# Optimization experiments

Measured on AMD Instinct MI355X. Metric: run time of the kernel, lower is better.

## Reference

```python
import jax, jax.numpy as jnp
import numpy as np

B, N, D_ATOM, HID, L = 32, 64, 5, 256, 9
E = N * N
F_E = 2 * HID + 2  # [h_i, h_j, d^2, edge_attr]


def _gather(x, idx):
    # x: (B, N, D), idx: (B, E) -> (B, E, D)
    return jax.vmap(lambda a, i: a[i])(x, idx)


def _segsum(data, idx, n):
    # per-batch unsorted segment sum over destination node idx
    return jax.vmap(lambda d, i: jax.ops.segment_sum(d, i, num_segments=n))(data, idx)


def _safe_dist(diff):
    # sqrt of squared norm, safe at 0 (masked self-edges) for grads
    return jnp.sqrt(jnp.maximum(jnp.sum(diff ** 2, axis=-1, keepdims=True), 1e-12))


def _remove_mean(x, mask):
    n = jnp.sum(mask, axis=1, keepdims=True)
    return (x - jnp.sum(x, axis=1, keepdims=True) / n) * mask


def setup_inputs() -> dict:
    key = jax.random.key(0)
    ks = iter(jax.random.split(key, 32))

    def W(shape):
        return jax.random.normal(next(ks), shape, jnp.float32) * 0.02

    x_in = jax.random.normal(next(ks), (B, N, 3), jnp.float32)
    h_in = jax.random.uniform(next(ks), (B, N, D_ATOM), dtype=jnp.float32)
    t = jax.random.uniform(next(ks), (B, N, 1), dtype=jnp.float32)
    ii, jj = jnp.meshgrid(jnp.arange(N), jnp.arange(N), indexing='ij')
    edges = jnp.stack([ii.reshape(-1), jj.reshape(-1)], axis=-1).astype(jnp.int32)  # (E,2) all pairs
    edge_indices = jnp.broadcast_to(edges[None], (B, E, 2))
    node_mask = jnp.ones((B, N, 1), jnp.float32)
    em = (edges[:, 0] != edges[:, 1]).astype(jnp.float32)[:, None]  # mask self-edges
    edge_mask = jnp.broadcast_to(em[None], (B, E, 1))
    params = dict(
        win_w=W((D_ATOM + 1, HID)), win_b=jnp.zeros((HID,), jnp.float32),
        wout_w=W((HID, D_ATOM + 1)), wout_b=jnp.zeros((D_ATOM + 1,), jnp.float32),
        we_w1=W((L, F_E, HID)), we_b1=jnp.zeros((L, HID), jnp.float32),
        we_w2=W((L, HID, HID)), we_b2=jnp.zeros((L, HID), jnp.float32),
        attn_w=W((L, HID, 1)), attn_b=jnp.zeros((L, 1), jnp.float32),
        wh_w1=W((L, 2 * HID, HID)), wh_b1=jnp.zeros((L, HID), jnp.float32),
        wh_w2=W((L, HID, HID)), wh_b2=jnp.zeros((L, HID), jnp.float32),
        wx_w1=W((L, F_E, HID)), wx_b1=jnp.zeros((L, HID), jnp.float32),
        wx_w2=W((L, HID, HID)), wx_b2=jnp.zeros((L, HID), jnp.float32),
        wx_w3=W((L, HID, 1)),
    )
    return dict(x_in=x_in, h_in=h_in, t=t, node_mask=node_mask, edge_mask=edge_mask,
                edge_indices=edge_indices, **params)


def reference(x_in, h_in, t, node_mask, edge_mask, edge_indices,
              win_w, win_b, wout_w, wout_b,
              we_w1, we_b1, we_w2, we_b2, attn_w, attn_b,
              wh_w1, wh_b1, wh_w2, wh_b2,
              wx_w1, wx_b1, wx_w2, wx_b2, wx_w3):
    idx_i = edge_indices[..., 0]
    idx_j = edge_indices[..., 1]
    # fixed edge attribute: initial pairwise distance
    d_in = _safe_dist(_gather(x_in, idx_i) - _gather(x_in, idx_j)) * edge_mask
    h0 = jnp.concatenate([h_in, t], axis=-1) @ win_w + win_b

    def block(carry, p):
        x, h = carry
        ew1, eb1, ew2, eb2, aw, ab, hw1, hb1, hw2, hb2, xw1, xb1, xw2, xb2, xw3 = p
        diff = (_gather(x, idx_i) - _gather(x, idx_j)) * edge_mask  # (B,E,3)
        d = _safe_dist(diff)  # (B,E,1)
        feat = jnp.concatenate([_gather(h, idx_i), _gather(h, idx_j), d ** 2, d_in], axis=-1) * edge_mask
        # edge MLP + attention gate, aggregated to node i
        m = jax.nn.silu(jax.nn.silu(feat @ ew1 + eb1) @ ew2 + eb2)
        em_agg = _segsum(jax.nn.sigmoid(m @ aw + ab) * m, idx_i, N)
        h_new = (h + (jax.nn.silu(jnp.concatenate([h, em_agg], axis=-1) @ hw1 + hb1) @ hw2 + hb2)) * node_mask
        # coordinate update (no bias on last layer)
        s = jax.nn.silu(jax.nn.silu(feat @ xw1 + xb1) @ xw2 + xb2) @ xw3  # (B,E,1)
        x_new = (x + _segsum(diff / (d + 1.0) * s, idx_i, N)) * node_mask
        return (x_new, h_new), None

    stacked = (we_w1, we_b1, we_w2, we_b2, attn_w, attn_b,
               wh_w1, wh_b1, wh_w2, wh_b2, wx_w1, wx_b1, wx_w2, wx_b2, wx_w3)
    (x, h), _ = jax.lax.scan(block, (x_in, h0), stacked)
    x_out = _remove_mean((x - x_in) * node_mask, node_mask)
    h_out = ((h @ wout_w + wout_b) * node_mask)[..., :-1]
    return jnp.concatenate([x_out, h_out], axis=-1)
```

## Files before the change

kernel.cpp:

```cpp
#include <hip/hip_runtime.h>
#include <hip/hip_bf16.h>
#include <math.h>


#define NB   32
#define NN   64
#define EPB  4096
#define HID  256
#define NL   9

typedef __attribute__((ext_vector_type(8))) short bfrag;
typedef __attribute__((ext_vector_type(4))) float f32x4;
typedef __attribute__((ext_vector_type(2))) float f32x2;

__device__ __forceinline__ float fast_rcp(float x) { return __builtin_amdgcn_rcpf(x); }
__device__ __forceinline__ float silu_f(float x) { return x * fast_rcp(1.f + __expf(-x)); }
__device__ __forceinline__ float sigm_f(float x) { return fast_rcp(1.f + __expf(-x)); }
__device__ __forceinline__ ushort bf16rne(float x) {
    unsigned u = __builtin_bit_cast(unsigned, x);
    u = (u + 0x7fffu + ((u >> 16) & 1u)) >> 16;
    return (ushort)u;
}
__device__ __forceinline__ float bf16tof(ushort h) {
    unsigned u = ((unsigned)h) << 16;
    return __builtin_bit_cast(float, u);
}
__device__ __forceinline__ unsigned pk2(f32x2 v) {
    float2 f; f.x = v.x; f.y = v.y;
    __hip_bfloat162 t = __float22bfloat162_rn(f);
    unsigned u;
    __builtin_memcpy(&u, &t, 4);
    return u;
}
__device__ __forceinline__ f32x2 fma2(f32x2 a, f32x2 b, f32x2 c) {
    return __builtin_elementwise_fma(a, b, c);
}
__device__ __forceinline__ f32x4 fma4(f32x4 a, f32x4 b, f32x4 c) {
    return __builtin_elementwise_fma(a, b, c);
}
__device__ __forceinline__ f32x2 silu2(f32x2 v) {
    f32x2 e = { __expf(-v.x), __expf(-v.y) };
    f32x2 d = e + (f32x2){1.f, 1.f};
    f32x2 r = { fast_rcp(d.x), fast_rcp(d.y) };
    return v * r;
}
__device__ __forceinline__ f32x4 silu4(f32x4 v) {
    f32x4 e = { __expf(-v.x), __expf(-v.y), __expf(-v.z), __expf(-v.w) };
    f32x4 d = e + (f32x4){1.f, 1.f, 1.f, 1.f};
    f32x4 r = { fast_rcp(d.x), fast_rcp(d.y), fast_rcp(d.z), fast_rcp(d.w) };
    return v * r;
}

__global__ void edm_k0_pre(const float* __restrict__ x_in, const float* __restrict__ h_in,
                           const float* __restrict__ t_in,
                           const float* __restrict__ win_w, const float* __restrict__ win_b,
                           float* __restrict__ h0, float* __restrict__ din_ws,
                           float* __restrict__ x0)
{
    int blk = blockIdx.x, tid = threadIdx.x;
    if (blk < NB * NN) {
        int node = blk;
        float acc = win_b[tid];
        #pragma unroll
        for (int k = 0; k < 5; ++k) acc += h_in[node * 5 + k] * win_w[k * HID + tid];
        acc += t_in[node] * win_w[5 * HID + tid];
        h0[node * HID + tid] = acc;
    } else if (blk < NB * NN + 512) {
        int e = (blk - NB * NN) * 256 + tid;
        int b = e >> 12, r = e & 4095, i = r >> 6, j = r & 63;
        const float* xb = x_in + b * NN * 3;
        float d0 = xb[i*3+0] - xb[j*3+0];
        float d1 = xb[i*3+1] - xb[j*3+1];
        float d2 = xb[i*3+2] - xb[j*3+2];
        float ss = d0*d0 + d1*d1 + d2*d2;
        float d  = sqrtf(fmaxf(ss, 1e-12f));
        din_ws[e] = (i != j) ? d : 0.f;
    } else {
        int idx = (blk - (NB * NN + 512)) * 256 + tid;
        if (idx < NB * NN * 3) x0[idx] = x_in[idx];
    }
}

__global__ void edm_k5_prep(const float* __restrict__ we_w2, const float* __restrict__ wx_w2,
                            ushort* __restrict__ W2Te, ushort* __restrict__ W2Tx)
{
    __shared__ float t_s[64][65];
    int blk = blockIdx.x;
    int mat = blk / 144, rem = blk % 144, l = rem >> 4, tile = rem & 15;
    int kt = tile >> 2, nt = tile & 3;
    const float* src = (mat ? wx_w2 : we_w2) + l * HID * HID;
    ushort* dst = (mat ? W2Tx : W2Te) + l * HID * HID;
    int col = threadIdx.x & 63, rg = threadIdx.x >> 6;
    #pragma unroll
    for (int it = 0; it < 16; ++it) {
        int row = rg * 16 + it;
        t_s[row][col] = src[(kt * 64 + row) * HID + nt * 64 + col];
    }
    __syncthreads();
    #pragma unroll
    for (int it = 0; it < 16; ++it) {
        int n = rg * 16 + it;
        dst[(nt * 64 + n) * HID + kt * 64 + col] = bf16rne(t_s[col][n]);
    }
}

__global__ void edm_k5b_prep(const float* __restrict__ we_w1, const float* __restrict__ wx_w1,
                             ushort* __restrict__ W1Th, ushort* __restrict__ W1Tl)
{
    __shared__ float t_s[64][65];
    int blk = blockIdx.x;
    int tile = blk & 15, out = (blk >> 4) & 3, l = blk >> 6;
    int kt = tile >> 2, nt = tile & 3;
    const float* src = ((out >= 2) ? wx_w1 : we_w1) + l * 514 * HID + (out & 1) * 256 * HID;
    size_t doff = ((size_t)(l * 4 + out)) * HID * HID;
    ushort* dh = W1Th + doff;
    ushort* dl = W1Tl + doff;
    int col = threadIdx.x & 63, rg = threadIdx.x >> 6;
    #pragma unroll
    for (int it = 0; it < 16; ++it) {
        int row = rg * 16 + it;
        t_s[row][col] = src[(kt * 64 + row) * HID + nt * 64 + col];
    }
    __syncthreads();
    #pragma unroll
    for (int it = 0; it < 16; ++it) {
        int n = rg * 16 + it;
        float v = t_s[col][n];
        ushort h = bf16rne(v);
        float lo = v - bf16tof(h);
        dh[(nt * 64 + n) * HID + kt * 64 + col] = h;
        dl[(nt * 64 + n) * HID + kt * 64 + col] = bf16rne(lo);
    }
}

__global__ void edm_k5c_prep(const float* __restrict__ wh_w1, const float* __restrict__ wh_w2,
                             ushort* __restrict__ W3h, ushort* __restrict__ W3l,
                             ushort* __restrict__ W4h, ushort* __restrict__ W4l)
{
    __shared__ float t_s[64][65];
    int blk = blockIdx.x;
    const float* src; ushort* dh; ushort* dl; int kt, nt, Kdim;
    if (blk < 288) {
        int l = blk >> 5, tile = blk & 31;
        kt = tile >> 2; nt = tile & 3; Kdim = 512;
        src = wh_w1 + (size_t)l * 512 * HID;
        dh = W3h + (size_t)l * HID * 512;
        dl = W3l + (size_t)l * HID * 512;
    } else {
        int b2 = blk - 288;
        int l = b2 >> 4, tile = b2 & 15;
        kt = tile >> 2; nt = tile & 3; Kdim = 256;
        src = wh_w2 + (size_t)l * HID * HID;
        dh = W4h + (size_t)l * HID * HID;
        dl = W4l + (size_t)l * HID * HID;
    }
    int col = threadIdx.x & 63, rg = threadIdx.x >> 6;
    #pragma unroll
    for (int it = 0; it < 16; ++it) {
        int row = rg * 16 + it;
        t_s[row][col] = src[(size_t)(kt * 64 + row) * HID + nt * 64 + col];
    }
    __syncthreads();
    #pragma unroll
    for (int it = 0; it < 16; ++it) {
        int n = rg * 16 + it;
        float v = t_s[col][n];
        ushort h = bf16rne(v);
        float lo = v - bf16tof(h);
        dh[(size_t)(nt * 64 + n) * Kdim + kt * 64 + col] = h;
        dl[(size_t)(nt * 64 + n) * Kdim + kt * 64 + col] = bf16rne(lo);
    }
}

__global__ __launch_bounds__(256)
void edm_k1_mfma(const float* __restrict__ h,
                 const ushort* __restrict__ W1Th, const ushort* __restrict__ W1Tl,
                 const float* __restrict__ we_b1, const float* __restrict__ wx_b1,
                 const float* __restrict__ we_w2, const float* __restrict__ we_b2,
                 const float* __restrict__ attn_w, const float* __restrict__ attn_b,
                 float* __restrict__ HeA, float* __restrict__ HeB,
                 float* __restrict__ HxA, float* __restrict__ HxB,
                 float* __restrict__ self_em, int l)
{
    int tid = threadIdx.x;
    if (blockIdx.x == 512) {
        __shared__ float m1s[HID];
        __shared__ float ms[HID];
        __shared__ float wred[4];
        __shared__ float gsh;
        const float* eb1 = we_b1 + l * HID;
        m1s[tid] = silu_f(eb1[tid]);
        __syncthreads();
        const float* W2 = we_w2 + l * HID * HID;
        float acc = we_b2[l * HID + tid];
        for (int k = 0; k < HID; ++k) acc += m1s[k] * W2[k * HID + tid];
        float mv = silu_f(acc);
        ms[tid] = mv;
        float p = mv * attn_w[l * HID + tid];
        #pragma unroll
        for (int off = 32; off > 0; off >>= 1) p += __shfl_down(p, off, 64);
        if ((tid & 63) == 0) wred[tid >> 6] = p;
        __syncthreads();
        if (tid == 0) gsh = sigm_f(wred[0] + wred[1] + wred[2] + wred[3] + attn_b[l]);
        __syncthreads();
        self_em[tid] = gsh * ms[tid];
        return;
    }

    __shared__ __align__(16) ushort Ah_s[16384];
    __shared__ __align__(16) ushort Al_s[16384];

    const int cq = blockIdx.x & 3;
    const int out = (blockIdx.x >> 2) & 3;
    const int ntile = blockIdx.x >> 4;
    const int base = ntile * 64;

    {
        const int c  = tid & 31;
        const int jg = tid >> 5;
        const int k0 = c * 8;
        #pragma unroll
        for (int it = 0; it < 8; ++it) {
            int m = it * 8 + jg;
            f32x4 h0 = *(const f32x4*)&h[(base + m) * HID + k0];
            f32x4 h1 = *(const f32x4*)&h[(base + m) * HID + k0 + 4];
            uint4 phi, plo;
            {
                ushort ax = bf16rne(h0.x), ay = bf16rne(h0.y);
                phi.x = (unsigned)ax | ((unsigned)ay << 16);
                plo.x = pk2((f32x2){h0.x - bf16tof(ax), h0.y - bf16tof(ay)});
            }
            {
                ushort ax = bf16rne(h0.z), ay = bf16rne(h0.w);
                phi.y = (unsigned)ax | ((unsigned)ay << 16);
                plo.y = pk2((f32x2){h0.z - bf16tof(ax), h0.w - bf16tof(ay)});
            }
            {
                ushort ax = bf16rne(h1.x), ay = bf16rne(h1.y);
                phi.z = (unsigned)ax | ((unsigned)ay << 16);
                plo.z = pk2((f32x2){h1.x - bf16tof(ax), h1.y - bf16tof(ay)});
            }
            {
                ushort ax = bf16rne(h1.z), ay = bf16rne(h1.w);
                phi.w = (unsigned)ax | ((unsigned)ay << 16);
                plo.w = pk2((f32x2){h1.z - bf16tof(ax), h1.w - bf16tof(ay)});
            }
            unsigned off = (unsigned)(m * 256 + ((c ^ (m & 7)) * 8));
            *(uint4*)&Ah_s[off] = phi;
            *(uint4*)&Al_s[off] = plo;
        }
    }
    __syncthreads();

    const int w = tid >> 6, lane = tid & 63, quad = lane >> 4, l16 = lane & 15;
    const int col = cq * 64 + w * 16 + l16;
    const ushort* Bh = W1Th + ((size_t)(l * 4 + out)) * HID * HID + (size_t)col * HID;
    const ushort* Bl = W1Tl + ((size_t)(l * 4 + out)) * HID * HID + (size_t)col * HID;

    f32x4 acc[4];
    #pragma unroll
    for (int mt = 0; mt < 4; ++mt) acc[mt] = (f32x4){0.f, 0.f, 0.f, 0.f};

    #pragma unroll
    for (int kt = 0; kt < 8; ++kt) {
        const int kof = kt * 32 + quad * 8;
        const int ch  = (kt * 4 + quad) ^ (l16 & 7);
        bfrag bh = *(const bfrag*)&Bh[kof];
        bfrag bl = *(const bfrag*)&Bl[kof];
        bfrag ahr[4], alr[4];
        #pragma unroll
        for (int mt = 0; mt < 4; ++mt) {
            ahr[mt] = *(const bfrag*)&Ah_s[(mt * 16 + l16) * 256 + ch * 8];
            alr[mt] = *(const bfrag*)&Al_s[(mt * 16 + l16) * 256 + ch * 8];
        }
        #pragma unroll
        for (int mt = 0; mt < 4; ++mt) {
            acc[mt] = __builtin_amdgcn_mfma_f32_16x16x32_bf16(ahr[mt], bh, acc[mt], 0, 0, 0);
            acc[mt] = __builtin_amdgcn_mfma_f32_16x16x32_bf16(ahr[mt], bl, acc[mt], 0, 0, 0);
            acc[mt] = __builtin_amdgcn_mfma_f32_16x16x32_bf16(alr[mt], bh, acc[mt], 0, 0, 0);
        }
    }

    float bias = 0.f;
    if (out == 0) bias = we_b1[l * HID + col];
    else if (out == 2) bias = wx_b1[l * HID + col];
    float* dst = (out == 0) ? HeA : (out == 1) ? HeB : (out == 2) ? HxA : HxB;
    #pragma unroll
    for (int mt = 0; mt < 4; ++mt)
        #pragma unroll
        for (int r = 0; r < 4; ++r)
            dst[(base + mt * 16 + quad * 4 + r) * HID + col] = acc[mt][r] + bias;
}

__global__ __launch_bounds__(256, 4)
void edm_kb_gemm(const float* __restrict__ x_cur, float* __restrict__ x_next,
                 const float* __restrict__ HeA, const float* __restrict__ HeB,
                 const float* __restrict__ HxA, const float* __restrict__ HxB,
                 const float* __restrict__ din_ws,
                 const float* __restrict__ we_w1, const float* __restrict__ we_b1,
                 const float* __restrict__ wx_w1, const float* __restrict__ wx_b1,
                 const ushort* __restrict__ W2Te, const ushort* __restrict__ W2Tx,
                 const float* __restrict__ we_b2, const float* __restrict__ wx_b2,
                 const float* __restrict__ attn_w, const float* __restrict__ attn_b,
                 const float* __restrict__ wx_w3,
                 float* __restrict__ em_agg, int l)
{
    __shared__ __align__(16) ushort A_s[16384];
    __shared__ float red_s[256];
    __shared__ float sc_s[64];
    __shared__ float x_s[192];
    __shared__ float d2_s[64], din_s[64];

    const int tid = threadIdx.x;
    const int blk = blockIdx.x;
    const int p = blk >> 11, bi = blk & 2047, b = bi >> 6, i = bi & 63;

    if (tid < 192) x_s[tid] = x_cur[b * 192 + tid];
    __syncthreads();
    if (tid < 64) {
        int j = tid;
        float d0 = x_s[i*3+0] - x_s[j*3+0];
        float d1 = x_s[i*3+1] - x_s[j*3+1];
        float d2 = x_s[i*3+2] - x_s[j*3+2];
        float ss = d0*d0 + d1*d1 + d2*d2;
        float d  = sqrtf(fmaxf(ss, 1e-12f));
        d2_s[j]  = d * d;
        din_s[j] = din_ws[b * EPB + i * 64 + j];
    }
    __syncthreads();

    {
        const float* W1  = (p ? wx_w1 : we_w1) + l * 514 * HID;
        const float* HA  = (p ? HxA : HeA);
        const float* HB  = (p ? HxB : HeB);
        const float* b1p = (p ? wx_b1 : we_b1) + l * HID;

        const int c  = tid & 31;
        const int jg = tid >> 5;
        const int k0 = c * 8;

        f32x4 ra0 = *(const f32x4*)&HA[(b * 64 + i) * HID + k0];
        f32x4 ra1 = *(const f32x4*)&HA[(b * 64 + i) * HID + k0 + 4];
        f32x4 wa0 = *(const f32x4*)&W1[512 * HID + k0];
        f32x4 wa1 = *(const f32x4*)&W1[512 * HID + k0 + 4];
        f32x4 wb0 = *(const f32x4*)&W1[513 * HID + k0];
        f32x4 wb1 = *(const f32x4*)&W1[513 * HID + k0 + 4];
        f32x4 b10 = *(const f32x4*)&b1p[k0];
        f32x4 b11 = *(const f32x4*)&b1p[k0 + 4];
        uint4 pki;
        pki.x = pk2(silu2((f32x2){b10.x, b10.y}));
        pki.y = pk2(silu2((f32x2){b10.z, b10.w}));
        pki.z = pk2(silu2((f32x2){b11.x, b11.y}));
        pki.w = pk2(silu2((f32x2){b11.z, b11.w}));

        const float* hbp = HB + b * 64 * HID + k0;
        #pragma unroll
        for (int it = 0; it < 8; ++it) {
            int j = it * 8 + jg;
            f32x4 h0 = *(const f32x4*)&hbp[j * HID];
            f32x4 h1 = *(const f32x4*)&hbp[j * HID + 4];
            f32x2 dd = { d2_s[j], d2_s[j] };
            f32x2 dn = { din_s[j], din_s[j] };
            uint4 pkv;
            f32x2 v;
            v = fma2(dn, (f32x2){wb0.x, wb0.y},
                 fma2(dd, (f32x2){wa0.x, wa0.y},
                      (f32x2){ra0.x + h0.x, ra0.y + h0.y}));
            pkv.x = pk2(silu2(v));
            v = fma2(dn, (f32x2){wb0.z, wb0.w},
                 fma2(dd, (f32x2){wa0.z, wa0.w},
                      (f32x2){ra0.z + h0.z, ra0.w + h0.w}));
            pkv.y = pk2(silu2(v));
            v = fma2(dn, (f32x2){wb1.x, wb1.y},
                 fma2(dd, (f32x2){wa1.x, wa1.y},
                      (f32x2){ra1.x + h1.x, ra1.y + h1.y}));
            pkv.z = pk2(silu2(v));
            v = fma2(dn, (f32x2){wb1.z, wb1.w},
                 fma2(dd, (f32x2){wa1.z, wa1.w},
                      (f32x2){ra1.z + h1.z, ra1.w + h1.w}));
            pkv.w = pk2(silu2(v));
            if (j == i) pkv = pki;
            *(uint4*)&A_s[j * 256 + (unsigned)((c ^ (j & 7)) * 8)] = pkv;
        }
    }
    __syncthreads();

    const int w = tid >> 6, lane = tid & 63, quad = lane >> 4, l16 = lane & 15;
    const ushort* W2T = (p ? W2Tx : W2Te) + l * HID * HID;
    const int cb0 = w * 64 + l16;
    f32x4 acc[4][4];
    #pragma unroll
    for (int mt = 0; mt < 4; ++mt)
        #pragma unroll
        for (int nt = 0; nt < 4; ++nt) acc[mt][nt] = (f32x4){0.f, 0.f, 0.f, 0.f};

    #pragma unroll
    for (int kt = 0; kt < 8; ++kt) {
        const int kof = kt * 32 + quad * 8;
        const int ch  = (kt * 4 + quad) ^ (l16 & 7);
        bfrag bfr[4], afr[4];
        #pragma unroll
        for (int nt = 0; nt < 4; ++nt)
            bfr[nt] = *(const bfrag*)&W2T[(cb0 + nt * 16) * HID + kof];
        #pragma unroll
        for (int mt = 0; mt < 4; ++mt)
            afr[mt] = *(const bfrag*)&A_s[(mt * 16 + l16) * 256 + ch * 8];
        #pragma unroll
        for (int mt = 0; mt < 4; ++mt)
            #pragma unroll
            for (int nt = 0; nt < 4; ++nt)
                acc[mt][nt] = __builtin_amdgcn_mfma_f32_16x16x32_bf16(
                    afr[mt], bfr[nt], acc[mt][nt], 0, 0, 0);
    }

    const float* b2p = (p ? wx_b2 : we_b2) + l * HID;
    const float* vvp = p ? (wx_w3 + l * HID) : (attn_w + l * HID);
    float b2v[4], vv[4];
    #pragma unroll
    for (int nt = 0; nt < 4; ++nt) { b2v[nt] = b2p[cb0 + nt * 16]; vv[nt] = vvp[cb0 + nt * 16]; }

    #pragma unroll
    for (int mt = 0; mt < 4; ++mt)
        #pragma unroll
        for (int nt = 0; nt < 4; ++nt) {
            f32x4 bb = { b2v[nt], b2v[nt], b2v[nt], b2v[nt] };
            acc[mt][nt] = silu4(acc[mt][nt] + bb);
        }

    #pragma unroll
    for (int mt = 0; mt < 4; ++mt) {
        f32x4 t4 = acc[mt][0] * (f32x4){vv[0], vv[0], vv[0], vv[0]};
        t4 = fma4(acc[mt][1], (f32x4){vv[1], vv[1], vv[1], vv[1]}, t4);
        t4 = fma4(acc[mt][2], (f32x4){vv[2], vv[2], vv[2], vv[2]}, t4);
        t4 = fma4(acc[mt][3], (f32x4){vv[3], vv[3], vv[3], vv[3]}, t4);
        #pragma unroll
        for (int r = 0; r < 4; ++r) {
            float pd = t4[r];
            pd += __shfl_xor(pd, 1, 64); pd += __shfl_xor(pd, 2, 64);
            pd += __shfl_xor(pd, 4, 64); pd += __shfl_xor(pd, 8, 64);
            if (l16 == 0) red_s[w * 64 + mt * 16 + quad * 4 + r] = pd;
        }
    }
    __syncthreads();
    if (tid < 64) {
        float tot = red_s[tid] + red_s[64 + tid] + red_s[128 + tid] + red_s[192 + tid];
        if (p == 0) sc_s[tid] = (tid == i) ? 0.f : sigm_f(tot + attn_b[l]);
        else        sc_s[tid] = tot;
    }
    __syncthreads();

    if (p == 0) {
        f32x4 g[4];
        #pragma unroll
        for (int mt = 0; mt < 4; ++mt) g[mt] = *(const f32x4*)&sc_s[mt * 16 + quad * 4];
        #pragma unroll
        for (int nt = 0; nt < 4; ++nt) {
            f32x4 e4 = g[0] * acc[0][nt];
            e4 = fma4(g[1], acc[1][nt], e4);
            e4 = fma4(g[2], acc[2][nt], e4);
            e4 = fma4(g[3], acc[3][nt], e4);
            float e = (e4.x + e4.y) + (e4.z + e4.w);
            e += __shfl_xor(e, 16, 64); e += __shfl_xor(e, 32, 64);
            if (quad == 0) em_agg[(b * 64 + i) * HID + cb0 + nt * 16] = e;
        }
    } else {
        if (tid < 64) {
            int j = tid;
            float d0 = x_s[i*3+0] - x_s[j*3+0];
            float d1 = x_s[i*3+1] - x_s[j*3+1];
            float d2 = x_s[i*3+2] - x_s[j*3+2];
            float ss = d0*d0 + d1*d1 + d2*d2;
            float d  = sqrtf(fmaxf(ss, 1e-12f));
            float f  = fast_rcp(d + 1.f) * sc_s[j];
            float cx = d0 * f, cy = d1 * f, cz = d2 * f;
            #pragma unroll
            for (int off = 32; off > 0; off >>= 1) {
                cx += __shfl_down(cx, off, 64);
                cy += __shfl_down(cy, off, 64);
                cz += __shfl_down(cz, off, 64);
            }
            if (tid == 0) {
                x_next[bi * 3 + 0] = x_s[i*3+0] + cx;
                x_next[bi * 3 + 1] = x_s[i*3+1] + cy;
                x_next[bi * 3 + 2] = x_s[i*3+2] + cz;
            }
        }
    }
}

__global__ __launch_bounds__(256)
void edm_k3a(const float* __restrict__ h, const float* __restrict__ em_agg,
             const float* __restrict__ self_em,
             const ushort* __restrict__ W3h, const ushort* __restrict__ W3l,
             const float* __restrict__ wh_b1,
             ushort* __restrict__ Uh, ushort* __restrict__ Ul, int l)
{
    __shared__ __align__(16) ushort Ah_s[16 * 512];
    __shared__ __align__(16) ushort Al_s[16 * 512];

    const int tid = threadIdx.x;
    const int cq = blockIdx.x & 3;
    const int base = (blockIdx.x >> 2) * 16;

    {
        const int c  = tid & 63;
        const int jg = tid >> 6;
        const int k0 = c * 8;
        #pragma unroll
        for (int t = 0; t < 4; ++t) {
            int m = t * 4 + jg;
            f32x4 v0, v1;
            if (c < 32) {
                v0 = *(const f32x4*)&h[(base + m) * HID + k0];
                v1 = *(const f32x4*)&h[(base + m) * HID + k0 + 4];
            } else {
                int e0 = k0 - 256;
                f32x4 a0 = *(const f32x4*)&em_agg[(base + m) * HID + e0];
                f32x4 a1 = *(const f32x4*)&em_agg[(base + m) * HID + e0 + 4];
                f32x4 s0 = *(const f32x4*)&self_em[e0];
                f32x4 s1 = *(const f32x4*)&self_em[e0 + 4];
                v0 = a0 + s0; v1 = a1 + s1;
            }
            uint4 phi, plo;
            {
                ushort ax = bf16rne(v0.x), ay = bf16rne(v0.y);
                phi.x = (unsigned)ax | ((unsigned)ay << 16);
                plo.x = pk2((f32x2){v0.x - bf16tof(ax), v0.y - bf16tof(ay)});
            }
            {
                ushort ax = bf16rne(v0.z), ay = bf16rne(v0.w);
                phi.y = (unsigned)ax | ((unsigned)ay << 16);
                plo.y = pk2((f32x2){v0.z - bf16tof(ax), v0.w - bf16tof(ay)});
            }
            {
                ushort ax = bf16rne(v1.x), ay = bf16rne(v1.y);
                phi.z = (unsigned)ax | ((unsigned)ay << 16);
                plo.z = pk2((f32x2){v1.x - bf16tof(ax), v1.y - bf16tof(ay)});
            }
            {
                ushort ax = bf16rne(v1.z), ay = bf16rne(v1.w);
                phi.w = (unsigned)ax | ((unsigned)ay << 16);
                plo.w = pk2((f32x2){v1.z - bf16tof(ax), v1.w - bf16tof(ay)});
            }
            unsigned off = (unsigned)(m * 512 + ((c ^ (m & 7)) * 8));
            *(uint4*)&Ah_s[off] = phi;
            *(uint4*)&Al_s[off] = plo;
        }
    }
    __syncthreads();

    const int w = tid >> 6, lane = tid & 63, quad = lane >> 4, l16 = lane & 15;
    const int colv = cq * 64 + w * 16 + l16;

    f32x4 acc = (f32x4){0.f, 0.f, 0.f, 0.f};
    const ushort* Bh = W3h + ((size_t)l * HID + colv) * 512;
    const ushort* Bl = W3l + ((size_t)l * HID + colv) * 512;

    for (int ks = 0; ks < 16; ++ks) {
        const int kof = ks * 32 + quad * 8;
        unsigned aoff = (unsigned)(l16 * 512 + (((ks * 4 + quad) ^ (l16 & 7))) * 8);
        bfrag ah = *(const bfrag*)&Ah_s[aoff];
        bfrag al = *(const bfrag*)&Al_s[aoff];
        bfrag bh = *(const bfrag*)&Bh[kof];
        bfrag bl = *(const bfrag*)&Bl[kof];
        acc = __builtin_amdgcn_mfma_f32_16x16x32_bf16(ah, bh, acc, 0, 0, 0);
        acc = __builtin_amdgcn_mfma_f32_16x16x32_bf16(ah, bl, acc, 0, 0, 0);
        acc = __builtin_amdgcn_mfma_f32_16x16x32_bf16(al, bh, acc, 0, 0, 0);
    }

    float b1v = wh_b1[l * HID + colv];
    #pragma unroll
    for (int r = 0; r < 4; ++r) {
        float u = silu_f(acc[r] + b1v);
        ushort uh = bf16rne(u);
        float ulo = u - bf16tof(uh);
        int row = quad * 4 + r;
        size_t ao = (size_t)(base + row) * 256 + (((colv >> 3) ^ (row & 7))) * 8 + (colv & 7);
        Uh[ao] = uh;
        Ul[ao] = bf16rne(ulo);
    }
}

__global__ __launch_bounds__(256)
void edm_k3b(const float* __restrict__ h,
             const ushort* __restrict__ Uh, const ushort* __restrict__ Ul,
             const ushort* __restrict__ W4h, const ushort* __restrict__ W4l,
             const float* __restrict__ wh_b2,
             float* __restrict__ h_next, int l)
{
    const int tid = threadIdx.x;
    const int cq = blockIdx.x & 3;
    const int base = (blockIdx.x >> 2) * 16;
    const int w = tid >> 6, lane = tid & 63, quad = lane >> 4, l16 = lane & 15;
    const int colv = cq * 64 + w * 16 + l16;

    const ushort* Bh = W4h + ((size_t)l * HID + colv) * HID;
    const ushort* Bl = W4l + ((size_t)l * HID + colv) * HID;
    const ushort* Ah = Uh + (size_t)(base + l16) * 256;
    const ushort* Al = Ul + (size_t)(base + l16) * 256;

    f32x4 acc = (f32x4){0.f, 0.f, 0.f, 0.f};
    #pragma unroll
    for (int kt = 0; kt < 8; ++kt) {
        const int kof = kt * 32 + quad * 8;
        unsigned ach = (unsigned)((((kt * 4 + quad) ^ (l16 & 7))) * 8);
        bfrag ah = *(const bfrag*)&Ah[ach];
        bfrag al = *(const bfrag*)&Al[ach];
        bfrag bh = *(const bfrag*)&Bh[kof];
        bfrag bl = *(const bfrag*)&Bl[kof];
        acc = __builtin_amdgcn_mfma_f32_16x16x32_bf16(ah, bh, acc, 0, 0, 0);
        acc = __builtin_amdgcn_mfma_f32_16x16x32_bf16(ah, bl, acc, 0, 0, 0);
        acc = __builtin_amdgcn_mfma_f32_16x16x32_bf16(al, bh, acc, 0, 0, 0);
    }

    float b2v = wh_b2[l * HID + colv];
    #pragma unroll
    for (int r = 0; r < 4; ++r) {
        int node = base + quad * 4 + r;
        h_next[node * HID + colv] = h[node * HID + colv] + acc[r] + b2v;
    }
}

__global__ void edm_k4_out(const float* __restrict__ x_fin, const float* __restrict__ x_in,
                           const float* __restrict__ h_fin,
                           const float* __restrict__ wout_w, const float* __restrict__ wout_b,
                           float* __restrict__ out)
{
    __shared__ float vx[192];
    __shared__ float mean_s[3];
    int b = blockIdx.x, tid = threadIdx.x;
    if (tid < 192) vx[tid] = x_fin[b * 192 + tid] - x_in[b * 192 + tid];
    __syncthreads();
    if (tid < 3) {
        float s = 0.f;
        for (int n = 0; n < 64; ++n) s += vx[n * 3 + tid];
        mean_s[tid] = s * (1.f / 64.f);
    }
    __syncthreads();
    if (tid < 192) out[b * 512 + (tid / 3) * 8 + (tid % 3)] = vx[tid] - mean_s[tid % 3];

    int node = tid / 5, ch = tid % 5;
    float acc = wout_b[ch];
    const float* hr = h_fin + (b * 64 + node) * HID;
    for (int k = 0; k < HID; ++k) acc = fmaf(hr[k], wout_w[k * 6 + ch], acc);
    out[b * 512 + node * 8 + 3 + ch] = acc;
}

extern "C" void kernel_launch(void* const* d_in, const int* in_sizes, int n_in,
                              void* d_out, int out_size, void* d_ws, size_t ws_size,
                              hipStream_t stream)
{
    const float* x_in   = (const float*)d_in[0];
    const float* h_in   = (const float*)d_in[1];
    const float* t_in   = (const float*)d_in[2];
    const float* win_w  = (const float*)d_in[6];
    const float* win_b  = (const float*)d_in[7];
    const float* wout_w = (const float*)d_in[8];
    const float* wout_b = (const float*)d_in[9];
    const float* we_w1  = (const float*)d_in[10];
    const float* we_b1  = (const float*)d_in[11];
    const float* we_w2  = (const float*)d_in[12];
    const float* we_b2  = (const float*)d_in[13];
    const float* attn_w = (const float*)d_in[14];
    const float* attn_b = (const float*)d_in[15];
    const float* wh_w1  = (const float*)d_in[16];
    const float* wh_b1  = (const float*)d_in[17];
    const float* wh_w2  = (const float*)d_in[18];
    const float* wh_b2  = (const float*)d_in[19];
    const float* wx_w1  = (const float*)d_in[20];
    const float* wx_b1  = (const float*)d_in[21];
    const float* wx_w2  = (const float*)d_in[22];
    const float* wx_b2  = (const float*)d_in[23];
    const float* wx_w3  = (const float*)d_in[24];

    float* ws = (float*)d_ws;
    const size_t SN = (size_t)NB * NN * HID;
    float* h_a = ws;
    float* h_b = ws + SN;
    float* HeA = ws + 2 * SN;
    float* HeB = ws + 3 * SN;
    float* HxA = ws + 4 * SN;
    float* HxB = ws + 5 * SN;
    float* emg = ws + 6 * SN;
    float* din = ws + 7 * SN;
    float* x_a = din + (size_t)NB * EPB;
    float* x_b = x_a + NB * NN * 3;
    float* sem = x_b + NB * NN * 3;
    ushort* W2Te = (ushort*)(sem + 256);
    ushort* W2Tx = W2Te + (size_t)NL * HID * HID;
    ushort* W1Th = W2Tx + (size_t)NL * HID * HID;
    ushort* W1Tl = W1Th + (size_t)NL * 4 * HID * HID;
    ushort* W3h  = W1Tl + (size_t)NL * 4 * HID * HID;
    ushort* W3l  = W3h + (size_t)NL * HID * 512;
    ushort* W4h  = W3l + (size_t)NL * HID * 512;
    ushort* W4l  = W4h + (size_t)NL * HID * HID;
    ushort* Uh   = W4l + (size_t)NL * HID * HID;
    ushort* Ul   = Uh + (size_t)NB * NN * HID;

    edm_k5_prep<<<dim3(288), dim3(256), 0, stream>>>(we_w2, wx_w2, W2Te, W2Tx);
    edm_k5b_prep<<<dim3(576), dim3(256), 0, stream>>>(we_w1, wx_w1, W1Th, W1Tl);
    edm_k5c_prep<<<dim3(432), dim3(256), 0, stream>>>(wh_w1, wh_w2, W3h, W3l, W4h, W4l);

    edm_k0_pre<<<dim3(NB * NN + 512 + 24), dim3(256), 0, stream>>>(
        x_in, h_in, t_in, win_w, win_b, h_a, din, x_a);

    for (int l = 0; l < NL; ++l) {
        float* h_cur = (l & 1) ? h_b : h_a;
        float* h_nxt = (l & 1) ? h_a : h_b;
        float* x_cur = (l & 1) ? x_b : x_a;
        float* x_nxt = (l & 1) ? x_a : x_b;

        edm_k1_mfma<<<dim3(513), dim3(256), 0, stream>>>(
            h_cur, W1Th, W1Tl, we_b1, wx_b1, we_w2, we_b2, attn_w, attn_b,
            HeA, HeB, HxA, HxB, sem, l);

        edm_kb_gemm<<<dim3(2 * NB * NN), dim3(256), 0, stream>>>(
            x_cur, x_nxt, HeA, HeB, HxA, HxB, din,
            we_w1, we_b1, wx_w1, wx_b1, W2Te, W2Tx,
            we_b2, wx_b2, attn_w, attn_b, wx_w3, emg, l);

        edm_k3a<<<dim3(512), dim3(256), 0, stream>>>(
            h_cur, emg, sem, W3h, W3l, wh_b1, Uh, Ul, l);

        edm_k3b<<<dim3(512), dim3(256), 0, stream>>>(
            h_cur, Uh, Ul, W4h, W4l, wh_b2, h_nxt, l);
    }

    edm_k4_out<<<dim3(NB), dim3(320), 0, stream>>>(
        x_b, x_in, h_b, wout_w, wout_b, (float*)d_out);
}
```

Before: 1.199 ms.

## Split edge GEMM blocks across two j-halves with partial aggregation buffers

Each edge-GEMM block now handles 32 neighbor rows instead of 64, which doubles the grid to 8192 blocks and halves LDS and accumulator usage. Partial attention-weighted sums and coordinate shifts go to two separate buffers. The em_agg halves are summed inside k3a, and the x update moves into extra blocks of k3b. Distances are computed per thread inline, which removes a setup barrier. The intent is more parallelism and occupancy, paid for with redundant HA/weight loads per block and extra global traffic for the partial results.

```diff
diff --git a/kernel.cpp b/kernel.cpp
--- a/kernel.cpp
+++ b/kernel.cpp
@@ -293,7 +293,7 @@
 }
 
 __global__ __launch_bounds__(256, 4)
-void edm_kb_gemm(const float* __restrict__ x_cur, float* __restrict__ x_next,
+void edm_kb_gemm(const float* __restrict__ x_cur,
                  const float* __restrict__ HeA, const float* __restrict__ HeB,
                  const float* __restrict__ HxA, const float* __restrict__ HxB,
                  const float* __restrict__ din_ws,
@@ -303,31 +303,20 @@
                  const float* __restrict__ we_b2, const float* __restrict__ wx_b2,
                  const float* __restrict__ attn_w, const float* __restrict__ attn_b,
                  const float* __restrict__ wx_w3,
-                 float* __restrict__ em_agg, int l)
-{
-    __shared__ __align__(16) ushort A_s[16384];
-    __shared__ float red_s[256];
-    __shared__ float sc_s[64];
+                 float* __restrict__ emg, float* __restrict__ sx, int l)
+{
+    __shared__ __align__(16) ushort A_s[32 * 256];
+    __shared__ float red_s[128];
+    __shared__ float sc_s[32];
     __shared__ float x_s[192];
-    __shared__ float d2_s[64], din_s[64];
 
     const int tid = threadIdx.x;
     const int blk = blockIdx.x;
-    const int p = blk >> 11, bi = blk & 2047, b = bi >> 6, i = bi & 63;
+    const int p = blk >> 12, rem = blk & 4095, bi = rem >> 1, mh = rem & 1;
+    const int b = bi >> 6, i = bi & 63;
+    const size_t SN = (size_t)NB * NN * HID;
 
     if (tid < 192) x_s[tid] = x_cur[b * 192 + tid];
-    __syncthreads();
-    if (tid < 64) {
-        int j = tid;
-        float d0 = x_s[i*3+0] - x_s[j*3+0];
-        float d1 = x_s[i*3+1] - x_s[j*3+1];
-        float d2 = x_s[i*3+2] - x_s[j*3+2];
-        float ss = d0*d0 + d1*d1 + d2*d2;
-        float d  = sqrtf(fmaxf(ss, 1e-12f));
-        d2_s[j]  = d * d;
-        din_s[j] = din_ws[b * EPB + i * 64 + j];
-    }
-    __syncthreads();
 
     {
         const float* W1  = (p ? wx_w1 : we_w1) + l * 514 * HID;
@@ -338,6 +327,10 @@
         const int c  = tid & 31;
         const int jg = tid >> 5;
         const int k0 = c * 8;
+
+        float xi0 = x_cur[b * 192 + i * 3 + 0];
+        float xi1 = x_cur[b * 192 + i * 3 + 1];
+        float xi2 = x_cur[b * 192 + i * 3 + 2];
 
         f32x4 ra0 = *(const f32x4*)&HA[(b * 64 + i) * HID + k0];
         f32x4 ra1 = *(const f32x4*)&HA[(b * 64 + i) * HID + k0 + 4];
@@ -355,12 +348,22 @@
 
         const float* hbp = HB + b * 64 * HID + k0;
         #pragma unroll
-        for (int it = 0; it < 8; ++it) {
-            int j = it * 8 + jg;
+        for (int it = 0; it < 4; ++it) {
+            int lj = it * 8 + jg;
+            int j  = mh * 32 + lj;
+            float xj0 = x_cur[b * 192 + j * 3 + 0];
+            float xj1 = x_cur[b * 192 + j * 3 + 1];
+            float xj2 = x_cur[b * 192 + j * 3 + 2];
+            float e0 = xi0 - xj0, e1 = xi1 - xj1, e2 = xi2 - xj2;
+            float ss = e0*e0 + e1*e1 + e2*e2;
+            float d  = sqrtf(fmaxf(ss, 1e-12f));
+            float d2v = d * d;
+            float dnv = din_ws[b * EPB + i * 64 + j];
+
             f32x4 h0 = *(const f32x4*)&hbp[j * HID];
             f32x4 h1 = *(const f32x4*)&hbp[j * HID + 4];
-            f32x2 dd = { d2_s[j], d2_s[j] };
-            f32x2 dn = { din_s[j], din_s[j] };
+            f32x2 dd = { d2v, d2v };
+            f32x2 dn = { dnv, dnv };
             uint4 pkv;
             f32x2 v;
             v = fma2(dn, (f32x2){wb0.x, wb0.y},
@@ -380,7 +383,7 @@
                       (f32x2){ra1.z + h1.z, ra1.w + h1.w}));
             pkv.w = pk2(silu2(v));
             if (j == i) pkv = pki;
-            *(uint4*)&A_s[j * 256 + (unsigned)((c ^ (j & 7)) * 8)] = pkv;
+            *(uint4*)&A_s[lj * 256 + (unsigned)((c ^ (lj & 7)) * 8)] = pkv;
         }
     }
     __syncthreads();
@@ -388,9 +391,9 @@
     const int w = tid >> 6, lane = tid & 63, quad = lane >> 4, l16 = lane & 15;
     const ushort* W2T = (p ? W2Tx : W2Te) + l * HID * HID;
     const int cb0 = w * 64 + l16;
-    f32x4 acc[4][4];
-    #pragma unroll
-    for (int mt = 0; mt < 4; ++mt)
+    f32x4 acc[2][4];
+    #pragma unroll
+    for (int mt = 0; mt < 2; ++mt)
         #pragma unroll
         for (int nt = 0; nt < 4; ++nt) acc[mt][nt] = (f32x4){0.f, 0.f, 0.f, 0.f};
 
@@ -398,15 +401,15 @@
     for (int kt = 0; kt < 8; ++kt) {
         const int kof = kt * 32 + quad * 8;
         const int ch  = (kt * 4 + quad) ^ (l16 & 7);
-        bfrag bfr[4], afr[4];
+        bfrag bfr[4], afr[2];
         #pragma unroll
         for (int nt = 0; nt < 4; ++nt)
             bfr[nt] = *(const bfrag*)&W2T[(cb0 + nt * 16) * HID + kof];
         #pragma unroll
-        for (int mt = 0; mt < 4; ++mt)
+        for (int mt = 0; mt < 2; ++mt)
             afr[mt] = *(const bfrag*)&A_s[(mt * 16 + l16) * 256 + ch * 8];
         #pragma unroll
-        for (int mt = 0; mt < 4; ++mt)
+        for (int mt = 0; mt < 2; ++mt)
             #pragma unroll
             for (int nt = 0; nt < 4; ++nt)
                 acc[mt][nt] = __builtin_amdgcn_mfma_f32_16x16x32_bf16(
@@ -420,7 +423,7 @@
     for (int nt = 0; nt < 4; ++nt) { b2v[nt] = b2p[cb0 + nt * 16]; vv[nt] = vvp[cb0 + nt * 16]; }
 
     #pragma unroll
-    for (int mt = 0; mt < 4; ++mt)
+    for (int mt = 0; mt < 2; ++mt)
         #pragma unroll
         for (int nt = 0; nt < 4; ++nt) {
             f32x4 bb = { b2v[nt], b2v[nt], b2v[nt], b2v[nt] };
@@ -428,7 +431,7 @@
         }
 
     #pragma unroll
-    for (int mt = 0; mt < 4; ++mt) {
+    for (int mt = 0; mt < 2; ++mt) {
         f32x4 t4 = acc[mt][0] * (f32x4){vv[0], vv[0], vv[0], vv[0]};
         t4 = fma4(acc[mt][1], (f32x4){vv[1], vv[1], vv[1], vv[1]}, t4);
         t4 = fma4(acc[mt][2], (f32x4){vv[2], vv[2], vv[2], vv[2]}, t4);
@@ -438,58 +441,57 @@
             float pd = t4[r];
             pd += __shfl_xor(pd, 1, 64); pd += __shfl_xor(pd, 2, 64);
             pd += __shfl_xor(pd, 4, 64); pd += __shfl_xor(pd, 8, 64);
-            if (l16 == 0) red_s[w * 64 + mt * 16 + quad * 4 + r] = pd;
-        }
-    }
-    __syncthreads();
-    if (tid < 64) {
-        float tot = red_s[tid] + red_s[64 + tid] + red_s[128 + tid] + red_s[192 + tid];
-        if (p == 0) sc_s[tid] = (tid == i) ? 0.f : sigm_f(tot + attn_b[l]);
+            if (l16 == 0) red_s[w * 32 + mt * 16 + quad * 4 + r] = pd;
+        }
+    }
+    __syncthreads();
+    if (tid < 32) {
+        float tot = red_s[tid] + red_s[32 + tid] + red_s[64 + tid] + red_s[96 + tid];
+        int j = mh * 32 + tid;
+        if (p == 0) sc_s[tid] = (j == i) ? 0.f : sigm_f(tot + attn_b[l]);
         else        sc_s[tid] = tot;
     }
     __syncthreads();
 
     if (p == 0) {
-        f32x4 g[4];
-        #pragma unroll
-        for (int mt = 0; mt < 4; ++mt) g[mt] = *(const f32x4*)&sc_s[mt * 16 + quad * 4];
+        f32x4 g[2];
+        #pragma unroll
+        for (int mt = 0; mt < 2; ++mt) g[mt] = *(const f32x4*)&sc_s[mt * 16 + quad * 4];
         #pragma unroll
         for (int nt = 0; nt < 4; ++nt) {
             f32x4 e4 = g[0] * acc[0][nt];
             e4 = fma4(g[1], acc[1][nt], e4);
-            e4 = fma4(g[2], acc[2][nt], e4);
-            e4 = fma4(g[3], acc[3][nt], e4);
             float e = (e4.x + e4.y) + (e4.z + e4.w);
             e += __shfl_xor(e, 16, 64); e += __shfl_xor(e, 32, 64);
-            if (quad == 0) em_agg[(b * 64 + i) * HID + cb0 + nt * 16] = e;
+            if (quad == 0)
+                emg[mh * SN + (size_t)(b * 64 + i) * HID + cb0 + nt * 16] = e;
         }
     } else {
-        if (tid < 64) {
-            int j = tid;
+        if (tid < 32) {
+            int j = mh * 32 + tid;
             float d0 = x_s[i*3+0] - x_s[j*3+0];
             float d1 = x_s[i*3+1] - x_s[j*3+1];
             float d2 = x_s[i*3+2] - x_s[j*3+2];
             float ss = d0*d0 + d1*d1 + d2*d2;
             float d  = sqrtf(fmaxf(ss, 1e-12f));
-            float f  = fast_rcp(d + 1.f) * sc_s[j];
+            float f  = fast_rcp(d + 1.f) * sc_s[tid];
             float cx = d0 * f, cy = d1 * f, cz = d2 * f;
             #pragma unroll
-            for (int off = 32; off > 0; off >>= 1) {
+            for (int off = 16; off > 0; off >>= 1) {
                 cx += __shfl_down(cx, off, 64);
                 cy += __shfl_down(cy, off, 64);
                 cz += __shfl_down(cz, off, 64);
             }
             if (tid == 0) {
-                x_next[bi * 3 + 0] = x_s[i*3+0] + cx;
-                x_next[bi * 3 + 1] = x_s[i*3+1] + cy;
-                x_next[bi * 3 + 2] = x_s[i*3+2] + cz;
+                float* sxp = sx + (size_t)(mh * 2048 + bi) * 4;
+                sxp[0] = cx; sxp[1] = cy; sxp[2] = cz;
             }
         }
     }
 }
 
 __global__ __launch_bounds__(256)
-void edm_k3a(const float* __restrict__ h, const float* __restrict__ em_agg,
+void edm_k3a(const float* __restrict__ h, const float* __restrict__ emg,
              const float* __restrict__ self_em,
              const ushort* __restrict__ W3h, const ushort* __restrict__ W3l,
              const float* __restrict__ wh_b1,
@@ -501,6 +503,7 @@
     const int tid = threadIdx.x;
     const int cq = blockIdx.x & 3;
     const int base = (blockIdx.x >> 2) * 16;
+    const size_t SN = (size_t)NB * NN * HID;
 
     {
         const int c  = tid & 63;
@@ -515,11 +518,13 @@
                 v1 = *(const f32x4*)&h[(base + m) * HID + k0 + 4];
             } else {
                 int e0 = k0 - 256;
-                f32x4 a0 = *(const f32x4*)&em_agg[(base + m) * HID + e0];
-                f32x4 a1 = *(const f32x4*)&em_agg[(base + m) * HID + e0 + 4];
+                f32x4 a0 = *(const f32x4*)&emg[(size_t)(base + m) * HID + e0];
+                f32x4 a1 = *(const f32x4*)&emg[(size_t)(base + m) * HID + e0 + 4];
+                f32x4 c0 = *(const f32x4*)&emg[SN + (size_t)(base + m) * HID + e0];
+                f32x4 c1 = *(const f32x4*)&emg[SN + (size_t)(base + m) * HID + e0 + 4];
                 f32x4 s0 = *(const f32x4*)&self_em[e0];
                 f32x4 s1 = *(const f32x4*)&self_em[e0 + 4];
-                v0 = a0 + s0; v1 = a1 + s1;
+                v0 = (a0 + c0) + s0; v1 = (a1 + c1) + s1;
             }
             uint4 phi, plo;
             {
@@ -586,9 +591,23 @@
              const ushort* __restrict__ Uh, const ushort* __restrict__ Ul,
              const ushort* __restrict__ W4h, const ushort* __restrict__ W4l,
              const float* __restrict__ wh_b2,
-             float* __restrict__ h_next, int l)
+             float* __restrict__ h_next,
+             const float* __restrict__ x_cur, const float* __restrict__ sx,
+             float* __restrict__ x_next, int l)
 {
     const int tid = threadIdx.x;
+    if (blockIdx.x >= 512) {
+        int t = blockIdx.x - 512;
+        #pragma unroll
+        for (int s = 0; s < 3; ++s) {
+            int f = t * 768 + s * 256 + tid;
+            int node = f / 3, comp = f - node * 3;
+            x_next[f] = x_cur[f] + sx[(size_t)node * 4 + comp]
+                                 + sx[(size_t)(2048 + node) * 4 + comp];
+        }
+        return;
+    }
+
     const int cq = blockIdx.x & 3;
     const int base = (blockIdx.x >> 2) * 16;
     const int w = tid >> 6, lane = tid & 63, quad = lane >> 4, l16 = lane & 15;
@@ -682,11 +701,12 @@
     float* HxA = ws + 4 * SN;
     float* HxB = ws + 5 * SN;
     float* emg = ws + 6 * SN;
-    float* din = ws + 7 * SN;
+    float* din = ws + 8 * SN;
     float* x_a = din + (size_t)NB * EPB;
     float* x_b = x_a + NB * NN * 3;
     float* sem = x_b + NB * NN * 3;
-    ushort* W2Te = (ushort*)(sem + 256);
+    float* sx  = sem + 256;
+    ushort* W2Te = (ushort*)(sx + 2 * 2048 * 4);
     ushort* W2Tx = W2Te + (size_t)NL * HID * HID;
     ushort* W1Th = W2Tx + (size_t)NL * HID * HID;
     ushort* W1Tl = W1Th + (size_t)NL * 4 * HID * HID;
@@ -714,16 +734,16 @@
             h_cur, W1Th, W1Tl, we_b1, wx_b1, we_w2, we_b2, attn_w, attn_b,
             HeA, HeB, HxA, HxB, sem, l);
 
-        edm_kb_gemm<<<dim3(2 * NB * NN), dim3(256), 0, stream>>>(
-            x_cur, x_nxt, HeA, HeB, HxA, HxB, din,
+        edm_kb_gemm<<<dim3(2 * 4096), dim3(256), 0, stream>>>(
+            x_cur, HeA, HeB, HxA, HxB, din,
             we_w1, we_b1, wx_w1, wx_b1, W2Te, W2Tx,
-            we_b2, wx_b2, attn_w, attn_b, wx_w3, emg, l);
+            we_b2, wx_b2, attn_w, attn_b, wx_w3, emg, sx, l);
 
         edm_k3a<<<dim3(512), dim3(256), 0, stream>>>(
             h_cur, emg, sem, W3h, W3l, wh_b1, Uh, Ul, l);
 
-        edm_k3b<<<dim3(512), dim3(256), 0, stream>>>(
-            h_cur, Uh, Ul, W4h, W4l, wh_b2, h_nxt, l);
+        edm_k3b<<<dim3(520), dim3(256), 0, stream>>>(
+            h_cur, Uh, Ul, W4h, W4l, wh_b2, h_nxt, x_cur, sx, x_nxt, l);
     }
 
     edm_k4_out<<<dim3(NB), dim3(320), 0, stream>>>(
```

New measurement: 1.740 ms. 45.2% more time.
